# Kernel tuning notes

Hardware: AMD Instinct MI355X
Metric: run time of the kernel (lower is better)

## Reference

```python
import jax, jax.numpy as jnp
import numpy as np

N_NODES = 50000
N_EDGES = 800000
IN_FEATS = 9
H_FEATS = 64
HEADS = 3
N_CLASSES = 2
NEG_SLOPE = 0.2  # DGL GATConv default leaky_relu slope


def _gat_layer(x, src, dst, W, attn_l, attn_r, bias, n_nodes):
    """One DGL-style GATConv: returns [N, H, F_out] (pre head-sum)."""
    H, Fo = attn_l.shape
    feat = (x @ W).reshape(n_nodes, H, Fo)            # [N,H,Fo]
    el = jnp.einsum('nhf,hf->nh', feat, attn_l)        # [N,H]
    er = jnp.einsum('nhf,hf->nh', feat, attn_r)        # [N,H]
    e = jax.nn.leaky_relu(el[src] + er[dst], negative_slope=NEG_SLOPE)  # [E,H]
    # edge softmax over incoming edges per destination node
    m = jax.ops.segment_max(e, dst, num_segments=n_nodes)               # [N,H]
    ex = jnp.exp(e - m[dst])                                             # [E,H]
    s = jax.ops.segment_sum(ex, dst, num_segments=n_nodes)              # [N,H]
    alpha = ex / s[dst]                                                  # [E,H]
    # attention-weighted neighbor aggregation
    rst = jax.ops.segment_sum(alpha[:, :, None] * feat[src], dst,
                              num_segments=n_nodes)                      # [N,H,Fo]
    return rst + bias.reshape(1, H, Fo)


def setup_inputs() -> dict:
    key = jax.random.key(0)
    ks = jax.random.split(key, 16)
    feats = jax.random.normal(ks[0], (N_NODES, IN_FEATS), dtype=jnp.float32)
    src = jax.random.randint(ks[1], (N_EDGES,), 0, N_NODES, dtype=jnp.int32)
    dst = jax.random.randint(ks[2], (N_EDGES,), 0, N_NODES, dtype=jnp.int32)
    sc = 0.1
    # layer 1: in_feats -> H*H_FEATS
    W1 = jax.random.normal(ks[3], (IN_FEATS, HEADS * H_FEATS), dtype=jnp.float32) * sc
    al1 = jax.random.normal(ks[4], (HEADS, H_FEATS), dtype=jnp.float32) * sc
    ar1 = jax.random.normal(ks[5], (HEADS, H_FEATS), dtype=jnp.float32) * sc
    b1 = jnp.zeros((HEADS * H_FEATS,), dtype=jnp.float32)
    # middle block layer: H_FEATS -> H*H_FEATS
    W2 = jax.random.normal(ks[6], (H_FEATS, HEADS * H_FEATS), dtype=jnp.float32) * sc
    al2 = jax.random.normal(ks[7], (HEADS, H_FEATS), dtype=jnp.float32) * sc
    ar2 = jax.random.normal(ks[8], (HEADS, H_FEATS), dtype=jnp.float32) * sc
    b2 = jnp.zeros((HEADS * H_FEATS,), dtype=jnp.float32)
    # output layer: H_FEATS -> H*N_CLASSES
    W3 = jax.random.normal(ks[9], (H_FEATS, HEADS * N_CLASSES), dtype=jnp.float32) * sc
    al3 = jax.random.normal(ks[10], (HEADS, N_CLASSES), dtype=jnp.float32) * sc
    ar3 = jax.random.normal(ks[11], (HEADS, N_CLASSES), dtype=jnp.float32) * sc
    b3 = jnp.zeros((HEADS * N_CLASSES,), dtype=jnp.float32)
    return {"feats": feats, "src": src, "dst": dst,
            "W1": W1, "al1": al1, "ar1": ar1, "b1": b1,
            "W2": W2, "al2": al2, "ar2": ar2, "b2": b2,
            "W3": W3, "al3": al3, "ar3": ar3, "b3": b3}


def reference(feats, src, dst, W1, al1, ar1, b1, W2, al2, ar2, b2, W3, al3, ar3, b3):
    # dropout layers are identity at inference (in_dropout/feat_drop skipped)
    h = _gat_layer(feats, src, dst, W1, al1, ar1, b1, N_NODES).sum(axis=1)  # [N,H_FEATS]
    h = _gat_layer(h, src, dst, W2, al2, ar2, b2, N_NODES).sum(axis=1)       # [N,H_FEATS]
    o = _gat_layer(h, src, dst, W3, al3, ar3, b3, N_NODES).sum(axis=1)       # [N,N_CLASSES]
    return o
```

## Files before the change

### kernel.cpp

```cpp
#include <hip/hip_runtime.h>
#include <hip/hip_fp16.h>

#define N_NODES 50000
#define N_EDGES 800000
#define NBKT 196
#define BCAP 4480
#define EPB_BIN 4096
#define NB_BIN ((N_EDGES + EPB_BIN - 1) / EPB_BIN)
#define NB_EL 196
#define NB_PW 48

typedef _Float16 half8 __attribute__((ext_vector_type(8)));
typedef float f32x4 __attribute__((ext_vector_type(4)));

static __device__ __forceinline__ float lrelu(float x) { return fmaxf(x, 0.2f * x); }

static __device__ __forceinline__ float2 h2f(float bits) {
    union { float f; __half2 h; } u;
    u.f = bits;
    return __half22float2(u.h);
}
static __device__ __forceinline__ float f2h2(float a, float b) {
    union { float f; __half2 h; } u;
    u.h = __floats2half2_rn(a, b);
    return u.f;
}

__global__ void __launch_bounds__(256) k_front(const int* __restrict__ src,
                                               const int* __restrict__ dst,
                                               int* __restrict__ bfill,
                                               unsigned int* __restrict__ stage,
                                               const float* __restrict__ x,
                                               const float* __restrict__ W1,
                                               const float* __restrict__ al1,
                                               const float* __restrict__ ar1,
                                               float* __restrict__ xph,
                                               float* __restrict__ er,
                                               const float* __restrict__ W2,
                                               __half* __restrict__ Wt16,
                                               const float* __restrict__ al2,
                                               const float* __restrict__ ar2,
                                               float* __restrict__ Wa2,
                                               float* __restrict__ Wr2) {
    __shared__ int lcnt[NBKT];
    __shared__ int gb[NBKT];
    __shared__ int lf[NBKT];
    __shared__ float sWa[9 * 3];
    __shared__ float sWr[9 * 3];
    const int t = threadIdx.x;
    const int b = blockIdx.x;

    if (b < NB_BIN) {
        const int e0 = b * EPB_BIN;
        for (int i = t; i < NBKT; i += 256) lcnt[i] = 0;
        __syncthreads();
        int dcache[16];
#pragma unroll
        for (int i = 0; i < 16; ++i) {
            const int e = e0 + i * 256 + t;
            if (e < N_EDGES) {
                const int d = dst[e];
                dcache[i] = d;
                atomicAdd(&lcnt[d >> 8], 1);
            } else dcache[i] = -1;
        }
        __syncthreads();
        for (int i = t; i < NBKT; i += 256) {
            gb[i] = i * BCAP + atomicAdd(&bfill[i], lcnt[i]);
            lf[i] = 0;
        }
        __syncthreads();
#pragma unroll
        for (int i = 0; i < 16; ++i) {
            const int e = e0 + i * 256 + t;
            if (e < N_EDGES) {
                const int d = dcache[i];
                const int bk = d >> 8;
                const int r = atomicAdd(&lf[bk], 1);
                stage[gb[bk] + r] = (unsigned int)src[e] | ((unsigned int)(d & 255) << 16);
            }
        }
        return;
    }
    if (b < NB_BIN + NB_EL) {
        if (t < 27) {
            const int h = t / 9, k = t % 9;
            float sa = 0.f, sr = 0.f;
            for (int f = 0; f < 64; ++f) {
                const float w = W1[k * 192 + h * 64 + f];
                sa += w * al1[h * 64 + f];
                sr += w * ar1[h * 64 + f];
            }
            sWa[k * 3 + h] = sa;
            sWr[k * 3 + h] = sr;
        }
        __syncthreads();
        const int n = (b - NB_BIN) * 256 + t;
        if (n >= N_NODES) return;
        const float* __restrict__ xr = x + (size_t)n * 9;
        float xv[9];
        float a0 = 0.f, a1 = 0.f, a2 = 0.f, r0 = 0.f, r1 = 0.f, r2 = 0.f;
#pragma unroll
        for (int k = 0; k < 9; ++k) {
            xv[k] = xr[k];
            a0 += xv[k] * sWa[k * 3 + 0];
            a1 += xv[k] * sWa[k * 3 + 1];
            a2 += xv[k] * sWa[k * 3 + 2];
            r0 += xv[k] * sWr[k * 3 + 0];
            r1 += xv[k] * sWr[k * 3 + 1];
            r2 += xv[k] * sWr[k * 3 + 2];
        }
        float* __restrict__ xo = xph + (size_t)n * 8;
        *reinterpret_cast<float4*>(xo) = make_float4(a0, a1, a2, f2h2(xv[0], xv[1]));
        *reinterpret_cast<float4*>(xo + 4) =
            make_float4(f2h2(xv[2], xv[3]), f2h2(xv[4], xv[5]),
                        f2h2(xv[6], xv[7]), f2h2(xv[8], 0.f));
        *reinterpret_cast<float4*>(er + (size_t)n * 4) = make_float4(r0, r1, r2, 0.f);
        return;
    }
    if (b < NB_BIN + NB_EL + NB_PW) {
        const int idx = (b - (NB_BIN + NB_EL)) * 256 + t;
        if (idx < 64 * 192) {
            const int n = idx / 192, ke = idx % 192;
            Wt16[idx] = __float2half(W2[(ke & 63) * 192 + (ke >> 6) * 64 + n]);
        }
        return;
    }
    if (t < 192) {
        const int h = t >> 6, k = t & 63;
        float sa = 0.f, sr = 0.f;
        for (int f = 0; f < 64; ++f) {
            const float w = W2[k * 192 + h * 64 + f];
            sa += w * al2[h * 64 + f];
            sr += w * ar2[h * 64 + f];
        }
        Wa2[k * 4 + h] = sa;
        Wr2[k * 4 + h] = sr;
        if (h == 0) { Wa2[k * 4 + 3] = 0.f; Wr2[k * 4 + 3] = 0.f; }
    }
}

__global__ void __launch_bounds__(512) k_bscatter2(const unsigned int* __restrict__ stage,
                                                   const int* __restrict__ bfill,
                                                   int* __restrict__ rowp,
                                                   int* __restrict__ col) {
    __shared__ int lcnt[256];
    __shared__ int lpos[256];
    __shared__ int sexc[256];
    __shared__ int sscan[256];
    const int t = threadIdx.x;
    const int b = blockIdx.x;
    const int n0 = b << 8;
    int bv = 0;
    if (t < 256) {
        bv = (t < NBKT) ? bfill[t] : 0;
        sscan[t] = bv;
        lcnt[t] = 0;
    }
    __syncthreads();
    for (int off = 1; off < 256; off <<= 1) {
        int u = 0;
        if (t < 256 && t >= off) u = sscan[t - off];
        __syncthreads();
        if (t < 256) sscan[t] += u;
        __syncthreads();
    }
    const int base = (b == 0) ? 0 : sscan[b - 1];
    const int cnt = bfill[b];
    const unsigned int* __restrict__ st = stage + (size_t)b * BCAP;

    for (int j = t; j < cnt; j += 512)
        atomicAdd(&lcnt[(st[j] >> 16) & 255], 1);
    __syncthreads();
    int v = 0;
    if (t < 256) { v = lcnt[t]; lpos[t] = v; }
    __syncthreads();
    for (int off = 1; off < 256; off <<= 1) {
        int u = 0;
        if (t < 256 && t >= off) u = lpos[t - off];
        __syncthreads();
        if (t < 256) lpos[t] += u;
        __syncthreads();
    }
    if (t < 256) {
        sexc[t] = lpos[t] - v;
        if (n0 + t < N_NODES) rowp[n0 + t] = base + sexc[t];
        lcnt[t] = 0;
    }
    if (b == NBKT - 1 && t == 0) rowp[N_NODES] = N_EDGES;
    __syncthreads();
    for (int j = t; j < cnt; j += 512) {
        const unsigned int e = st[j];
        const int local = (int)(e >> 16) & 255;
        const int r = atomicAdd(&lcnt[local], 1);
        col[base + sexc[local] + r] = (int)(e & 0xFFFFu);
    }
}

__global__ void __launch_bounds__(256, 6) k_l1(const float* __restrict__ xph,
                                               const float* __restrict__ er_in,
                                               const int* __restrict__ rowp,
                                               const int* __restrict__ col,
                                               const float* __restrict__ W1,
                                               const float* __restrict__ b1,
                                               const float* __restrict__ Wa2,
                                               const float* __restrict__ Wr2,
                                               __half* __restrict__ hout,
                                               float* __restrict__ el,
                                               float* __restrict__ er_out) {
    __shared__ union {
        float At[16 * 28];
        float vbuf[16][72];
    } u;
    __shared__ float part[3][16][64];
    const int t = threadIdx.x;
    const int wv = t >> 6;
    const int lane = t & 63;
    const int q = lane >> 4;
    const int ql = lane & 15;
    const int li = wv * 4 + q;
    const int nbase = blockIdx.x * 16;
    const int n = nbase + li;
    const char* __restrict__ xb = (const char*)xph;

    {
        const int jb = rowp[n], je = rowp[n + 1];
        const float4 er4 = *reinterpret_cast<const float4*>(er_in + (size_t)n * 4);
        float acc[27];
#pragma unroll
        for (int j = 0; j < 27; ++j) acc[j] = 0.f;
        float sw0 = 0.f, sw1 = 0.f, sw2 = 0.f;

        for (int e = jb + ql; e < je; e += 32) {
            const int e2 = e + 16;
            const bool v2 = (e2 < je);
            const int off1 = col[e] << 5;
            const int off2 = (v2 ? col[e2] : col[e]) << 5;
            const float4 xa1 = *reinterpret_cast<const float4*>(xb + off1);
            const float4 xb1 = *reinterpret_cast<const float4*>(xb + off1 + 16);
            const float4 xa2 = *reinterpret_cast<const float4*>(xb + off2);
            const float4 xb2 = *reinterpret_cast<const float4*>(xb + off2 + 16);
            const float m2 = v2 ? 1.f : 0.f;
            const float w10 = __expf(lrelu(xa1.x + er4.x));
            const float w11 = __expf(lrelu(xa1.y + er4.y));
            const float w12 = __expf(lrelu(xa1.z + er4.z));
            const float w20 = __expf(lrelu(xa2.x + er4.x)) * m2;
            const float w21 = __expf(lrelu(xa2.y + er4.y)) * m2;
            const float w22 = __expf(lrelu(xa2.z + er4.z)) * m2;
            sw0 += w10 + w20; sw1 += w11 + w21; sw2 += w12 + w22;
            const float2 p10 = h2f(xa1.w), p11 = h2f(xb1.x), p12 = h2f(xb1.y),
                         p13 = h2f(xb1.z), p14 = h2f(xb1.w);
            const float2 p20 = h2f(xa2.w), p21 = h2f(xb2.x), p22 = h2f(xb2.y),
                         p23 = h2f(xb2.z), p24 = h2f(xb2.w);
            const float x1[9] = {p10.x, p10.y, p11.x, p11.y, p12.x, p12.y, p13.x, p13.y, p14.x};
            const float x2[9] = {p20.x, p20.y, p21.x, p21.y, p22.x, p22.y, p23.x, p23.y, p24.x};
#pragma unroll
            for (int k = 0; k < 9; ++k) {
                acc[0 + k]  += w10 * x1[k] + w20 * x2[k];
                acc[9 + k]  += w11 * x1[k] + w21 * x2[k];
                acc[18 + k] += w12 * x1[k] + w22 * x2[k];
            }
        }
#pragma unroll
        for (int off = 1; off < 16; off <<= 1) {
            sw0 += __shfl_xor(sw0, off);
            sw1 += __shfl_xor(sw1, off);
            sw2 += __shfl_xor(sw2, off);
#pragma unroll
            for (int j = 0; j < 27; ++j) acc[j] += __shfl_xor(acc[j], off);
        }
        if (ql == 0) {
            const bool has = (je > jb);
            const float i0 = has ? 1.f / sw0 : 0.f;
            const float i1 = has ? 1.f / sw1 : 0.f;
            const float i2 = has ? 1.f / sw2 : 0.f;
            float* __restrict__ ao = u.At + li * 28;
#pragma unroll
            for (int k = 0; k < 9; ++k) {
                ao[k] = acc[k] * i0;
                ao[9 + k] = acc[9 + k] * i1;
                ao[18 + k] = acc[18 + k] * i2;
            }
        }
    }
    __syncthreads();

    {
        const int h = wv;
        const int c = lane;
        if (h < 3) {
            float wreg[9];
#pragma unroll
            for (int k = 0; k < 9; ++k) wreg[k] = W1[k * 192 + h * 64 + c];
#pragma unroll
            for (int i = 0; i < 16; ++i) {
                const float* __restrict__ arp = u.At + i * 28 + h * 9;
                float acc = 0.f;
#pragma unroll
                for (int k = 0; k < 9; ++k) acc += arp[k] * wreg[k];
                part[h][i][c] = acc;
            }
        }
        __syncthreads();
        const float bsum = b1[c] + b1[64 + c] + b1[128 + c];
        for (int idx = t; idx < 1024; idx += 256) {
            const int i = idx >> 6, cc = idx & 63;
            const float v = part[0][i][cc] + part[1][i][cc] + part[2][i][cc] + bsum;
            hout[(size_t)(nbase + i) * 64 + cc] = __float2half(v);
            u.vbuf[i][cc] = v;
        }
        __syncthreads();
        if (t < 96) {
            const int i = t / 6, r = t % 6;
            const int h3 = (r < 3) ? r : r - 3;
            const float* __restrict__ tab = (r < 3) ? Wa2 : Wr2;
            float s = 0.f;
#pragma unroll 8
            for (int c2 = 0; c2 < 64; ++c2) s += u.vbuf[i][c2] * tab[c2 * 4 + h3];
            if (r < 3) el[(size_t)(nbase + i) * 4 + h3] = s;
            else       er_out[(size_t)(nbase + i) * 4 + h3] = s;
        }
    }
}

__global__ void __launch_bounds__(256, 8) k_aggw64(const __half* __restrict__ x,
                                                   const float* __restrict__ el,
                                                   const float* __restrict__ er,
                                                   const int* __restrict__ rowp,
                                                   const int* __restrict__ col,
                                                   __half* __restrict__ agg) {
    const int wv = threadIdx.x >> 6;
    const int lane = threadIdx.x & 63;
    const int n = blockIdx.x * 4 + wv;
    const int jb = rowp[n], je = rowp[n + 1];

    __shared__ float4 wbuf4[4][64];
    const float4 er4 = *reinterpret_cast<const float4*>(er + (size_t)n * 4);
    const int p = lane >> 5;
    const int foff = (lane & 31) * 4;
    const char* __restrict__ xbase = (const char*)x;
    const char* __restrict__ elbase = (const char*)el;
    float a00 = 0.f, a01 = 0.f, a02 = 0.f;
    float a10 = 0.f, a11 = 0.f, a12 = 0.f;
    float sw0 = 0.f, sw1 = 0.f, sw2 = 0.f;

    for (int c0 = jb; c0 < je; c0 += 64) {
        const int cnt = min(64, je - c0);
        if (lane < cnt) {
            const int s = col[c0 + lane];
            const float4 e4 = *reinterpret_cast<const float4*>(elbase + (s << 4));
            const float w0 = __expf(lrelu(e4.x + er4.x));
            const float w1 = __expf(lrelu(e4.y + er4.y));
            const float w2 = __expf(lrelu(e4.z + er4.z));
            wbuf4[wv][lane] = make_float4(w0, w1, w2, __int_as_float(s << 7));
            sw0 += w0; sw1 += w1; sw2 += w2;
        }
        __builtin_amdgcn_wave_barrier();
        int e = 0;
        for (; e + 4 <= cnt; e += 4) {
            const float4 q1 = wbuf4[wv][e + p];
            const float4 q2 = wbuf4[wv][e + 2 + p];
            const float2 f1 = __half22float2(*reinterpret_cast<const __half2*>(
                xbase + (__float_as_int(q1.w) + foff)));
            const float2 f2 = __half22float2(*reinterpret_cast<const __half2*>(
                xbase + (__float_as_int(q2.w) + foff)));
            a00 += q1.x * f1.x + q2.x * f2.x;
            a01 += q1.y * f1.x + q2.y * f2.x;
            a02 += q1.z * f1.x + q2.z * f2.x;
            a10 += q1.x * f1.y + q2.x * f2.y;
            a11 += q1.y * f1.y + q2.y * f2.y;
            a12 += q1.z * f1.y + q2.z * f2.y;
        }
        if (e + p < cnt) {
            const float4 q1 = wbuf4[wv][e + p];
            const float2 f1 = __half22float2(*reinterpret_cast<const __half2*>(
                xbase + (__float_as_int(q1.w) + foff)));
            a00 += q1.x * f1.x; a01 += q1.y * f1.x; a02 += q1.z * f1.x;
            a10 += q1.x * f1.y; a11 += q1.y * f1.y; a12 += q1.z * f1.y;
        }
        if (e + 2 + p < cnt) {
            const float4 q2 = wbuf4[wv][e + 2 + p];
            const float2 f2 = __half22float2(*reinterpret_cast<const __half2*>(
                xbase + (__float_as_int(q2.w) + foff)));
            a00 += q2.x * f2.x; a01 += q2.y * f2.x; a02 += q2.z * f2.x;
            a10 += q2.x * f2.y; a11 += q2.y * f2.y; a12 += q2.z * f2.y;
        }
    }
    a00 += __shfl_xor(a00, 32); a01 += __shfl_xor(a01, 32); a02 += __shfl_xor(a02, 32);
    a10 += __shfl_xor(a10, 32); a11 += __shfl_xor(a11, 32); a12 += __shfl_xor(a12, 32);
#pragma unroll
    for (int off = 32; off > 0; off >>= 1) {
        sw0 += __shfl_xor(sw0, off);
        sw1 += __shfl_xor(sw1, off);
        sw2 += __shfl_xor(sw2, off);
    }
    if (lane < 32) {
        const int f0 = (lane & 31) * 2;
        __half* __restrict__ ao = agg + (size_t)n * 192;
        if (je > jb) {
            const float i0 = 1.f / sw0, i1 = 1.f / sw1, i2 = 1.f / sw2;
            *reinterpret_cast<__half2*>(ao + f0) = __floats2half2_rn(a00 * i0, a10 * i0);
            *reinterpret_cast<__half2*>(ao + 64 + f0) = __floats2half2_rn(a01 * i1, a11 * i1);
            *reinterpret_cast<__half2*>(ao + 128 + f0) = __floats2half2_rn(a02 * i2, a12 * i2);
        } else {
            const __half2 z = __floats2half2_rn(0.f, 0.f);
            *reinterpret_cast<__half2*>(ao + f0) = z;
            *reinterpret_cast<__half2*>(ao + 64 + f0) = z;
            *reinterpret_cast<__half2*>(ao + 128 + f0) = z;
        }
    }
}

__global__ void __launch_bounds__(256) k_l23(const __half* __restrict__ aggH,
                                             const __half* __restrict__ Wt,
                                             const float* __restrict__ b2,
                                             const float* __restrict__ W3,
                                             const float* __restrict__ al3,
                                             const float* __restrict__ ar3,
                                             float* __restrict__ feat3p,
                                             float* __restrict__ er3) {
    __shared__ float xl[64 * 68];
    __shared__ float Wl[64 * 6];
    __shared__ float Wal[64 * 3];
    __shared__ float Wrl[64 * 3];
    const int t = threadIdx.x;
    const int n0 = blockIdx.x * 64;
    const int nvalid = min(64, N_NODES - n0);

    {
        const int wv = t >> 6;
        const int lane = t & 63;
        const int quad = lane >> 4;
        const int t16 = lane & 15;
        const int nwave = n0 + wv * 16;
        const int arow = min(nwave + t16, N_NODES - 1);
        half8 a[6];
#pragma unroll
        for (int kb = 0; kb < 6; ++kb)
            a[kb] = *reinterpret_cast<const half8*>(aggH + (size_t)arow * 192 + kb * 32 + quad * 8);
#pragma unroll
        for (int nt = 0; nt < 4; ++nt) {
            const int c = nt * 16 + t16;
            const float bs = b2[c] + b2[64 + c] + b2[128 + c];
            const __half* __restrict__ bt = Wt + (size_t)c * 192 + quad * 8;
            f32x4 acc = {0.f, 0.f, 0.f, 0.f};
#pragma unroll
            for (int kb = 0; kb < 6; ++kb) {
                const half8 bfr = *reinterpret_cast<const half8*>(bt + kb * 32);
                acc = __builtin_amdgcn_mfma_f32_16x16x32_f16(a[kb], bfr, acc, 0, 0, 0);
            }
#pragma unroll
            for (int r = 0; r < 4; ++r)
                xl[(wv * 16 + quad * 4 + r) * 68 + c] = acc[r] + bs;
        }
    }
    for (int idx = t; idx < 384; idx += 256) Wl[idx] = W3[idx];
    if (t < 192) {
        const int k = t & 63, h = t >> 6;
        Wal[k * 3 + h] = W3[k * 6 + h * 2] * al3[h * 2] + W3[k * 6 + h * 2 + 1] * al3[h * 2 + 1];
        Wrl[k * 3 + h] = W3[k * 6 + h * 2] * ar3[h * 2] + W3[k * 6 + h * 2 + 1] * ar3[h * 2 + 1];
    }
    __syncthreads();

#pragma unroll
    for (int hp = 0; hp < 2; ++hp) {
        const int i = (t >> 3) + hp * 32;
        const int slot = t & 7;
        if (i < nvalid && slot < 6) {
            float acc = 0.f;
#pragma unroll
            for (int k4 = 0; k4 < 16; ++k4) {
                const float4 xv = *reinterpret_cast<const float4*>(&xl[i * 68 + 4 * k4]);
                acc += Wl[(4 * k4 + 0) * 6 + slot] * xv.x;
                acc += Wl[(4 * k4 + 1) * 6 + slot] * xv.y;
                acc += Wl[(4 * k4 + 2) * 6 + slot] * xv.z;
                acc += Wl[(4 * k4 + 3) * 6 + slot] * xv.w;
            }
            reinterpret_cast<__half*>(feat3p + (size_t)(n0 + i) * 8)[6 + slot] = __float2half(acc);
        }
        if (t < 192) {
            const int ii = t / 6 + hp * 32, ss = t % 6;
            if (ii < nvalid) {
                const int hh = (ss < 3) ? ss : ss - 3;
                const float* __restrict__ wt = (ss < 3) ? Wal : Wrl;
                float acc = 0.f;
#pragma unroll 4
                for (int k = 0; k < 64; ++k) acc += xl[ii * 68 + k] * wt[k * 3 + hh];
                if (ss < 3) feat3p[(size_t)(n0 + ii) * 8 + hh] = acc;
                else        er3[(size_t)(n0 + ii) * 4 + hh] = acc;
            }
        }
    }
}

__global__ void __launch_bounds__(256, 4) k_agg3(const float* __restrict__ feat3p,
                                                 const float* __restrict__ er3,
                                                 const float* __restrict__ b3,
                                                 const int* __restrict__ rowp,
                                                 const int* __restrict__ col,
                                                 float* __restrict__ out) {
    const int tid = threadIdx.x;
    const int wv = tid >> 6;
    const int lane = tid & 63;
    const int q = lane >> 4;
    const int ql = lane & 15;
    const int n = (blockIdx.x * 4 + wv) * 4 + q;
    const int jb = rowp[n], je = rowp[n + 1];
    const float4 er4 = *reinterpret_cast<const float4*>(er3 + (size_t)n * 4);
    const char* __restrict__ fb = (const char*)feat3p;

    float acc[6];
#pragma unroll
    for (int j = 0; j < 6; ++j) acc[j] = 0.f;
    float sw0 = 0.f, sw1 = 0.f, sw2 = 0.f;

    for (int e = jb + ql; e < je; e += 64) {
        const int eb = e + 16, ec = e + 32, ed = e + 48;
        const bool vb = (eb < je), vc = (ec < je), vd = (ed < je);
        const int sa = col[e];
        const int offa = sa << 5;
        const int offb = (vb ? col[eb] : sa) << 5;
        const int offc = (vc ? col[ec] : sa) << 5;
        const int offd = (vd ? col[ed] : sa) << 5;
        const float4 fa1 = *reinterpret_cast<const float4*>(fb + offa);
        const float2 fb1 = *reinterpret_cast<const float2*>(fb + offa + 16);
        const float4 fa2 = *reinterpret_cast<const float4*>(fb + offb);
        const float2 fb2 = *reinterpret_cast<const float2*>(fb + offb + 16);
        const float4 fa3 = *reinterpret_cast<const float4*>(fb + offc);
        const float2 fb3 = *reinterpret_cast<const float2*>(fb + offc + 16);
        const float4 fa4 = *reinterpret_cast<const float4*>(fb + offd);
        const float2 fb4 = *reinterpret_cast<const float2*>(fb + offd + 16);
        const float mb = vb ? 1.f : 0.f, mc = vc ? 1.f : 0.f, md = vd ? 1.f : 0.f;
        const float w10 = __expf(lrelu(fa1.x + er4.x));
        const float w11 = __expf(lrelu(fa1.y + er4.y));
        const float w12 = __expf(lrelu(fa1.z + er4.z));
        const float w20 = __expf(lrelu(fa2.x + er4.x)) * mb;
        const float w21 = __expf(lrelu(fa2.y + er4.y)) * mb;
        const float w22 = __expf(lrelu(fa2.z + er4.z)) * mb;
        const float w30 = __expf(lrelu(fa3.x + er4.x)) * mc;
        const float w31 = __expf(lrelu(fa3.y + er4.y)) * mc;
        const float w32 = __expf(lrelu(fa3.z + er4.z)) * mc;
        const float w40 = __expf(lrelu(fa4.x + er4.x)) * md;
        const float w41 = __expf(lrelu(fa4.y + er4.y)) * md;
        const float w42 = __expf(lrelu(fa4.z + er4.z)) * md;
        sw0 += (w10 + w20) + (w30 + w40);
        sw1 += (w11 + w21) + (w31 + w41);
        sw2 += (w12 + w22) + (w32 + w42);
        const float2 f01a = h2f(fa1.w), f23a = h2f(fb1.x), f45a = h2f(fb1.y);
        const float2 f01b = h2f(fa2.w), f23b = h2f(fb2.x), f45b = h2f(fb2.y);
        const float2 f01c = h2f(fa3.w), f23c = h2f(fb3.x), f45c = h2f(fb3.y);
        const float2 f01d = h2f(fa4.w), f23d = h2f(fb4.x), f45d = h2f(fb4.y);
        acc[0] += (w10 * f01a.x + w20 * f01b.x) + (w30 * f01c.x + w40 * f01d.x);
        acc[1] += (w10 * f01a.y + w20 * f01b.y) + (w30 * f01c.y + w40 * f01d.y);
        acc[2] += (w11 * f23a.x + w21 * f23b.x) + (w31 * f23c.x + w41 * f23d.x);
        acc[3] += (w11 * f23a.y + w21 * f23b.y) + (w31 * f23c.y + w41 * f23d.y);
        acc[4] += (w12 * f45a.x + w22 * f45b.x) + (w32 * f45c.x + w42 * f45d.x);
        acc[5] += (w12 * f45a.y + w22 * f45b.y) + (w32 * f45c.y + w42 * f45d.y);
    }
#pragma unroll
    for (int off = 1; off < 16; off <<= 1) {
        sw0 += __shfl_xor(sw0, off);
        sw1 += __shfl_xor(sw1, off);
        sw2 += __shfl_xor(sw2, off);
#pragma unroll
        for (int j = 0; j < 6; ++j) acc[j] += __shfl_xor(acc[j], off);
    }
    if (ql == 0) {
        const bool has = (je > jb);
        const float i0 = has ? 1.f / sw0 : 0.f;
        const float i1 = has ? 1.f / sw1 : 0.f;
        const float i2 = has ? 1.f / sw2 : 0.f;
        const float o0 = acc[0] * i0 + acc[2] * i1 + acc[4] * i2 + b3[0] + b3[2] + b3[4];
        const float o1 = acc[1] * i0 + acc[3] * i1 + acc[5] * i2 + b3[1] + b3[3] + b3[5];
        *reinterpret_cast<float2*>(out + (size_t)n * 2) = make_float2(o0, o1);
    }
}

extern "C" void kernel_launch(void* const* d_in, const int* in_sizes, int n_in,
                              void* d_out, int out_size, void* d_ws, size_t ws_size,
                              hipStream_t stream) {
    const float* feats = (const float*)d_in[0];
    const int* src = (const int*)d_in[1];
    const int* dst = (const int*)d_in[2];
    const float* W1 = (const float*)d_in[3];
    const float* al1 = (const float*)d_in[4];
    const float* ar1 = (const float*)d_in[5];
    const float* b1 = (const float*)d_in[6];
    const float* W2 = (const float*)d_in[7];
    const float* al2 = (const float*)d_in[8];
    const float* ar2 = (const float*)d_in[9];
    const float* b2 = (const float*)d_in[10];
    const float* W3 = (const float*)d_in[11];
    const float* al3 = (const float*)d_in[12];
    const float* ar3 = (const float*)d_in[13];
    const float* b3 = (const float*)d_in[14];
    float* out = (float*)d_out;

    char* ws = (char*)d_ws;
    size_t off = 0;
    auto alloc = [&](size_t bytes) {
        void* p = ws + off;
        off += (bytes + 255) & ~(size_t)255;
        return p;
    };
    __half* aggH = (__half*)alloc((size_t)N_NODES * 192 * 2);
    __half* hbufH = (__half*)alloc((size_t)N_NODES * 64 * 2);
    float* xph = (float*)alloc((size_t)N_NODES * 8 * 4);
    float* el = (float*)alloc((size_t)N_NODES * 4 * 4);
    float* er = (float*)alloc((size_t)N_NODES * 4 * 4);
    int* bfill = (int*)alloc(256 * 4);
    int* rowp = (int*)alloc((size_t)(N_NODES + 1) * 4);
    int* col = (int*)alloc((size_t)N_EDGES * 4);
    unsigned int* stage = (unsigned int*)alloc((size_t)NBKT * BCAP * 4);
    __half* Wt16 = (__half*)alloc((size_t)64 * 192 * 2);
    float* Wa2 = (float*)alloc(256 * 4);
    float* Wr2 = (float*)alloc(256 * 4);
    float* feat3p = (float*)alloc((size_t)N_NODES * 8 * 4);
    (void)ws_size;

    const int ab = N_NODES / 4;
    const int qb = N_NODES / 16;
    const int lb = (N_NODES + 63) / 64;

    hipMemsetAsync(bfill, 0, 256 * 4, stream);
    k_front<<<NB_BIN + NB_EL + NB_PW + 1, 256, 0, stream>>>(
        src, dst, bfill, stage, feats, W1, al1, ar1, xph, er, W2, Wt16,
        al2, ar2, Wa2, Wr2);
    k_bscatter2<<<NBKT, 512, 0, stream>>>(stage, bfill, rowp, col);

    k_l1<<<qb, 256, 0, stream>>>(xph, er, rowp, col, W1, b1, Wa2, Wr2, hbufH, el, er);

    k_aggw64<<<ab, 256, 0, stream>>>(hbufH, el, er, rowp, col, aggH);

    k_l23<<<lb, 256, 0, stream>>>(aggH, Wt16, b2, W3, al3, ar3, feat3p, er);

    k_agg3<<<qb, 256, 0, stream>>>(feat3p, er, b3, rowp, col, out);
}
```

Before: 209.8 us.

## Map four destination nodes per wavefront in layer-2 aggregation with wider gathers

Restructures k_aggw64 so each 16-lane quarter-wave handles one destination node instead of a full wave per node, with each lane gathering 4 half features (8 bytes) per neighbor instead of 2. The aim is to cut idle lanes in the edge-weight phase (average degree is about 16, so 64-lane chunks were mostly empty) and issue fewer, wider gather loads with more edges in flight per lane. In exchange it uses more accumulator registers, hence the launch bounds drop to 6 waves, and adds load imbalance between the four nodes sharing a wave.

```diff
diff --git a/kernel.cpp b/kernel.cpp
--- a/kernel.cpp
+++ b/kernel.cpp
@@ -323,90 +323,103 @@
     }
 }
 
-__global__ void __launch_bounds__(256, 8) k_aggw64(const __half* __restrict__ x,
+__global__ void __launch_bounds__(256, 6) k_aggw64(const __half* __restrict__ x,
                                                    const float* __restrict__ el,
                                                    const float* __restrict__ er,
                                                    const int* __restrict__ rowp,
                                                    const int* __restrict__ col,
                                                    __half* __restrict__ agg) {
-    const int wv = threadIdx.x >> 6;
-    const int lane = threadIdx.x & 63;
-    const int n = blockIdx.x * 4 + wv;
+    const int t = threadIdx.x;
+    const int wv = t >> 6;
+    const int lane = t & 63;
+    const int q = lane >> 4;
+    const int ql = lane & 15;
+    const int n = (blockIdx.x * 4 + wv) * 4 + q;
     const int jb = rowp[n], je = rowp[n + 1];
 
-    __shared__ float4 wbuf4[4][64];
+    __shared__ float4 wbuf[4][4][16];
     const float4 er4 = *reinterpret_cast<const float4*>(er + (size_t)n * 4);
-    const int p = lane >> 5;
-    const int foff = (lane & 31) * 4;
     const char* __restrict__ xbase = (const char*)x;
     const char* __restrict__ elbase = (const char*)el;
-    float a00 = 0.f, a01 = 0.f, a02 = 0.f;
-    float a10 = 0.f, a11 = 0.f, a12 = 0.f;
+    const int foff = ql * 8;
+
+    float acc[12];
+#pragma unroll
+    for (int j = 0; j < 12; ++j) acc[j] = 0.f;
     float sw0 = 0.f, sw1 = 0.f, sw2 = 0.f;
 
-    for (int c0 = jb; c0 < je; c0 += 64) {
-        const int cnt = min(64, je - c0);
-        if (lane < cnt) {
-            const int s = col[c0 + lane];
+    for (int c0 = jb; c0 < je; c0 += 16) {
+        const int cnt = min(16, je - c0);
+        if (ql < cnt) {
+            const int s = col[c0 + ql];
             const float4 e4 = *reinterpret_cast<const float4*>(elbase + (s << 4));
             const float w0 = __expf(lrelu(e4.x + er4.x));
             const float w1 = __expf(lrelu(e4.y + er4.y));
             const float w2 = __expf(lrelu(e4.z + er4.z));
-            wbuf4[wv][lane] = make_float4(w0, w1, w2, __int_as_float(s << 7));
+            wbuf[wv][q][ql] = make_float4(w0, w1, w2, __int_as_float(s << 7));
             sw0 += w0; sw1 += w1; sw2 += w2;
         }
         __builtin_amdgcn_wave_barrier();
-        int e = 0;
-        for (; e + 4 <= cnt; e += 4) {
-            const float4 q1 = wbuf4[wv][e + p];
-            const float4 q2 = wbuf4[wv][e + 2 + p];
-            const float2 f1 = __half22float2(*reinterpret_cast<const __half2*>(
-                xbase + (__float_as_int(q1.w) + foff)));
-            const float2 f2 = __half22float2(*reinterpret_cast<const __half2*>(
-                xbase + (__float_as_int(q2.w) + foff)));
-            a00 += q1.x * f1.x + q2.x * f2.x;
-            a01 += q1.y * f1.x + q2.y * f2.x;
-            a02 += q1.z * f1.x + q2.z * f2.x;
-            a10 += q1.x * f1.y + q2.x * f2.y;
-            a11 += q1.y * f1.y + q2.y * f2.y;
-            a12 += q1.z * f1.y + q2.z * f2.y;
-        }
-        if (e + p < cnt) {
-            const float4 q1 = wbuf4[wv][e + p];
-            const float2 f1 = __half22float2(*reinterpret_cast<const __half2*>(
-                xbase + (__float_as_int(q1.w) + foff)));
-            a00 += q1.x * f1.x; a01 += q1.y * f1.x; a02 += q1.z * f1.x;
-            a10 += q1.x * f1.y; a11 += q1.y * f1.y; a12 += q1.z * f1.y;
-        }
-        if (e + 2 + p < cnt) {
-            const float4 q2 = wbuf4[wv][e + 2 + p];
-            const float2 f2 = __half22float2(*reinterpret_cast<const __half2*>(
-                xbase + (__float_as_int(q2.w) + foff)));
-            a00 += q2.x * f2.x; a01 += q2.y * f2.x; a02 += q2.z * f2.x;
-            a10 += q2.x * f2.y; a11 += q2.y * f2.y; a12 += q2.z * f2.y;
-        }
-    }
-    a00 += __shfl_xor(a00, 32); a01 += __shfl_xor(a01, 32); a02 += __shfl_xor(a02, 32);
-    a10 += __shfl_xor(a10, 32); a11 += __shfl_xor(a11, 32); a12 += __shfl_xor(a12, 32);
-#pragma unroll
-    for (int off = 32; off > 0; off >>= 1) {
+        int k = 0;
+        for (; k + 4 <= cnt; k += 4) {
+            const float4 q0 = wbuf[wv][q][k];
+            const float4 q1 = wbuf[wv][q][k + 1];
+            const float4 q2 = wbuf[wv][q][k + 2];
+            const float4 q3 = wbuf[wv][q][k + 3];
+            const float2 r0 = *reinterpret_cast<const float2*>(xbase + (__float_as_int(q0.w) + foff));
+            const float2 r1 = *reinterpret_cast<const float2*>(xbase + (__float_as_int(q1.w) + foff));
+            const float2 r2 = *reinterpret_cast<const float2*>(xbase + (__float_as_int(q2.w) + foff));
+            const float2 r3 = *reinterpret_cast<const float2*>(xbase + (__float_as_int(q3.w) + foff));
+            const float2 a01 = h2f(r0.x), a23 = h2f(r0.y);
+            const float2 b01 = h2f(r1.x), b23 = h2f(r1.y);
+            const float2 c01 = h2f(r2.x), c23 = h2f(r2.y);
+            const float2 d01 = h2f(r3.x), d23 = h2f(r3.y);
+            acc[0] += q0.x * a01.x + q1.x * b01.x + q2.x * c01.x + q3.x * d01.x;
+            acc[1] += q0.x * a01.y + q1.x * b01.y + q2.x * c01.y + q3.x * d01.y;
+            acc[2] += q0.x * a23.x + q1.x * b23.x + q2.x * c23.x + q3.x * d23.x;
+            acc[3] += q0.x * a23.y + q1.x * b23.y + q2.x * c23.y + q3.x * d23.y;
+            acc[4] += q0.y * a01.x + q1.y * b01.x + q2.y * c01.x + q3.y * d01.x;
+            acc[5] += q0.y * a01.y + q1.y * b01.y + q2.y * c01.y + q3.y * d01.y;
+            acc[6] += q0.y * a23.x + q1.y * b23.x + q2.y * c23.x + q3.y * d23.x;
+            acc[7] += q0.y * a23.y + q1.y * b23.y + q2.y * c23.y + q3.y * d23.y;
+            acc[8]  += q0.z * a01.x + q1.z * b01.x + q2.z * c01.x + q3.z * d01.x;
+            acc[9]  += q0.z * a01.y + q1.z * b01.y + q2.z * c01.y + q3.z * d01.y;
+            acc[10] += q0.z * a23.x + q1.z * b23.x + q2.z * c23.x + q3.z * d23.x;
+            acc[11] += q0.z * a23.y + q1.z * b23.y + q2.z * c23.y + q3.z * d23.y;
+        }
+        for (; k < cnt; ++k) {
+            const float4 q0 = wbuf[wv][q][k];
+            const float2 r0 = *reinterpret_cast<const float2*>(xbase + (__float_as_int(q0.w) + foff));
+            const float2 a01 = h2f(r0.x), a23 = h2f(r0.y);
+            acc[0] += q0.x * a01.x; acc[1] += q0.x * a01.y;
+            acc[2] += q0.x * a23.x; acc[3] += q0.x * a23.y;
+            acc[4] += q0.y * a01.x; acc[5] += q0.y * a01.y;
+            acc[6] += q0.y * a23.x; acc[7] += q0.y * a23.y;
+            acc[8]  += q0.z * a01.x; acc[9]  += q0.z * a01.y;
+            acc[10] += q0.z * a23.x; acc[11] += q0.z * a23.y;
+        }
+    }
+#pragma unroll
+    for (int off = 1; off < 16; off <<= 1) {
         sw0 += __shfl_xor(sw0, off);
         sw1 += __shfl_xor(sw1, off);
         sw2 += __shfl_xor(sw2, off);
     }
-    if (lane < 32) {
-        const int f0 = (lane & 31) * 2;
-        __half* __restrict__ ao = agg + (size_t)n * 192;
+    {
+        __half* __restrict__ ao = agg + (size_t)n * 192 + ql * 4;
         if (je > jb) {
             const float i0 = 1.f / sw0, i1 = 1.f / sw1, i2 = 1.f / sw2;
-            *reinterpret_cast<__half2*>(ao + f0) = __floats2half2_rn(a00 * i0, a10 * i0);
-            *reinterpret_cast<__half2*>(ao + 64 + f0) = __floats2half2_rn(a01 * i1, a11 * i1);
-            *reinterpret_cast<__half2*>(ao + 128 + f0) = __floats2half2_rn(a02 * i2, a12 * i2);
+            *reinterpret_cast<float2*>(ao) =
+                make_float2(f2h2(acc[0] * i0, acc[1] * i0), f2h2(acc[2] * i0, acc[3] * i0));
+            *reinterpret_cast<float2*>(ao + 64) =
+                make_float2(f2h2(acc[4] * i1, acc[5] * i1), f2h2(acc[6] * i1, acc[7] * i1));
+            *reinterpret_cast<float2*>(ao + 128) =
+                make_float2(f2h2(acc[8] * i2, acc[9] * i2), f2h2(acc[10] * i2, acc[11] * i2));
         } else {
-            const __half2 z = __floats2half2_rn(0.f, 0.f);
-            *reinterpret_cast<__half2*>(ao + f0) = z;
-            *reinterpret_cast<__half2*>(ao + 64 + f0) = z;
-            *reinterpret_cast<__half2*>(ao + 128 + f0) = z;
+            const float2 z = make_float2(f2h2(0.f, 0.f), f2h2(0.f, 0.f));
+            *reinterpret_cast<float2*>(ao) = z;
+            *reinterpret_cast<float2*>(ao + 64) = z;
+            *reinterpret_cast<float2*>(ao + 128) = z;
         }
     }
 }
@@ -618,7 +631,6 @@
     float* feat3p = (float*)alloc((size_t)N_NODES * 8 * 4);
     (void)ws_size;
 
-    const int ab = N_NODES / 4;
     const int qb = N_NODES / 16;
     const int lb = (N_NODES + 63) / 64;
 
@@ -630,7 +642,7 @@
 
     k_l1<<<qb, 256, 0, stream>>>(xph, er, rowp, col, W1, b1, Wa2, Wr2, hbufH, el, er);
 
-    k_aggw64<<<ab, 256, 0, stream>>>(hbufH, el, er, rowp, col, aggH);
+    k_aggw64<<<qb, 256, 0, stream>>>(hbufH, el, er, rowp, col, aggH);
 
     k_l23<<<lb, 256, 0, stream>>>(aggH, Wt16, b2, W3, al3, ar3, feat3p, er);
 
```

Result: faster. 202.9 us (-3.3%).
